# Kernel optimization log

Hardware: AMD Instinct MI355X
Metric: run time of the kernel (lower is better)

Reference implementation:

```python
import jax, jax.numpy as jnp
import numpy as np

C_IN = 4
C_OUT = 8
K = 5            # kernel_size (hardcoded by reshape(25,2) in original)
N_ROT = 8
R_B = 8          # rot_basis_size
STRIDE = 1
PAD = 2
TWO_PI = 2.0 * np.pi
ROT_SCALE = TWO_PI / R_B


def B2(x):
    # quadratic B-spline, exactly as in the torch source
    return (-3 * (-0.5 + x) ** 2 * jnp.sign(0.5 - x)
            + (-1.5 + x) ** 2 * jnp.sign(1.5 - x)
            - 3 * (1 + 2 * x) ** 2 * jnp.sign(0.5 + x) / 4
            + (3 + 2 * x) ** 2 * jnp.sign(1.5 + x) / 4) / 4


def angle_dist(th1, th2):
    return jnp.mod(th2 - th1 + np.pi, TWO_PI) - np.pi


def make_kernel_stack(weights):
    # weights: (C_IN, R_B*K*K, C_OUT). M = K*K*R_B combined (spatial-center, rot-center) index;
    # original repeats each spatial center R_B times (np.repeat) and tiles rot centers K*K times.
    lidx = -(K // 2)
    coords = jnp.arange(lidx, K // 2 + 1, dtype=jnp.float32)
    grid = jnp.stack(jnp.meshgrid(coords, coords, indexing='ij'), axis=-1)  # (K,K,2), grid[i,j]=[i+l, j+l]
    centers_xy = jnp.repeat(grid.reshape(K * K, 2), R_B, axis=0)            # (M,2)
    rot_centers = jnp.tile(jnp.arange(R_B, dtype=jnp.float32) * ROT_SCALE, K * K)  # (M,)
    rot_sample = jnp.arange(N_ROT, dtype=jnp.float32) * (TWO_PI / N_ROT)    # (N_ROT,)

    def one_kernel(theta):
        c, s = jnp.cos(theta), jnp.sin(theta)
        x, y = grid[..., 0], grid[..., 1]
        xxs = jnp.stack([x * c - y * s, x * s + y * c], axis=-1)            # (K,K,2) rotated sample grid
        xx_diffs = centers_xy[None, None, :, :] - xxs[:, :, None, :]        # (K,K,M,2)
        xx_vals = jnp.prod(B2(xx_diffs), axis=-1)                           # (K,K,M) separable spatial spline
        rots = rot_sample + theta                                           # (N_ROT,)
        rot_vals = B2(angle_dist(rots[:, None], rot_centers[None, :]) / ROT_SCALE)  # (N_ROT,M)
        vals = xx_vals[:, :, None, :] * rot_vals[None, None, :, :]          # (K,K,N_ROT,M)
        # contract basis index m against weights -> (C_OUT, C_IN, N_ROT, K, K)
        return jnp.einsum('xyrm,imo->oirxy', vals, weights)

    ks = jax.vmap(one_kernel)(-rot_sample)  # (N_ROT, C_OUT, C_IN, N_ROT, K, K), matches torch.cat over -theta
    return ks.reshape(N_ROT * C_OUT, C_IN * N_ROT, K, K)


def setup_inputs() -> dict:
    key = jax.random.key(0)
    kx, kw = jax.random.split(key)
    X = jax.random.normal(kx, (8, C_IN, N_ROT, 256, 256), dtype=jnp.float32)
    weights = jax.random.normal(kw, (C_IN, R_B * K * K, C_OUT), dtype=jnp.float32)
    return {'X': X, 'weights': weights}


def reference(X, weights):
    ks = make_kernel_stack(weights)                       # (N_ROT*C_OUT, C_IN*N_ROT, K, K)
    B, c, d, H, W = X.shape
    Xr = X.reshape(B, c * d, H, W)
    out = jax.lax.conv_general_dilated(
        Xr, ks, window_strides=(STRIDE, STRIDE),
        padding=[(PAD, PAD), (PAD, PAD)],
        dimension_numbers=('NCHW', 'OIHW', 'NCHW'))        # (B, N_ROT*C_OUT, h, w)
    Bn, _, h, w = out.shape
    out = out.reshape(Bn, N_ROT, C_OUT, h, w).transpose(0, 2, 1, 3, 4)  # (B, C_OUT, N_ROT, h, w)
    return (TWO_PI / N_ROT) * out
```

## Files before the change

### kernel.cpp

```cpp
#include <hip/hip_runtime.h>
#include <hip/hip_fp16.h>
#include <math.h>

#define PI_F      3.14159265358979323846f
#define TWO_PI_F  6.28318530717958647692f
#define PI4_F     0.78539816339744830962f

typedef _Float16 f16x8 __attribute__((ext_vector_type(8)));
typedef float    f32x4 __attribute__((ext_vector_type(4)));

__device__ __forceinline__ float sgn(float t) {
    return (t > 0.f) ? 1.f : ((t < 0.f) ? -1.f : 0.f);
}

__device__ __forceinline__ float b2(float x) {
    float a = x - 0.5f;
    float b = x - 1.5f;
    float c = 1.f + 2.f * x;
    float d = 3.f + 2.f * x;
    return (-3.f * a * a * sgn(0.5f - x)
            + b * b * sgn(1.5f - x)
            - 0.75f * c * c * sgn(0.5f + x)
            + 0.25f * d * d * sgn(1.5f + x)) * 0.25f;
}

__global__ void build_ks_kernel(const float* __restrict__ w, __half* __restrict__ ksh) {
    int g = blockIdx.x * 256 + threadIdx.x;
    if (g >= 64 * 32 * 25) return;
    int O = g & 63;
    int rest = g >> 6;
    int t = rest % 25;
    int I = rest / 25;
    int r0 = O >> 3, o = O & 7;
    int i = I >> 3, r = I & 7;
    int x = t / 5, y = t % 5;

    float theta = -(float)r0 * PI4_F;
    float cth = cosf(theta), sth = sinf(theta);
    float fx = (float)(x - 2), fy = (float)(y - 2);
    float xc = fx * cth - fy * sth;
    float yc = fx * sth + fy * cth;

    float rotv[8];
    float rs = (float)r * PI4_F + theta;
    #pragma unroll
    for (int mr = 0; mr < 8; ++mr) {
        float v = (float)mr * PI4_F - rs + PI_F;
        float md = fmodf(v, TWO_PI_F);
        if (md < 0.f) md += TWO_PI_F;
        rotv[mr] = b2((md - PI_F) / PI4_F);
    }

    float sum = 0.f;
    for (int mx = 0; mx < 25; ++mx) {
        float cx = (float)(mx / 5 - 2);
        float cy = (float)(mx % 5 - 2);
        float bx = b2(cx - xc) * b2(cy - yc);
        if (bx != 0.f) {
            const float* wp = w + (size_t)(i * 200 + mx * 8) * 8 + o;
            #pragma unroll
            for (int mr = 0; mr < 8; ++mr)
                sum = fmaf(bx * rotv[mr], wp[mr * 8], sum);
        }
    }
    ksh[(size_t)(t * 64 + O) * 32 + I] = __float2half(sum);
}

__global__ __launch_bounds__(256, 2) void conv_fused_kernel(const float* __restrict__ X,
                                                            const __half* __restrict__ ksh,
                                                            float* __restrict__ out) {
    __shared__ uint4 xt[4 * 721];

    int bid = blockIdx.x;
    int b   = bid >> 7;
    int rem = bid & 127;
    int h0  = (rem >> 3) << 4;
    int w0  = (rem & 7) << 5;
    int tid = threadIdx.x;

    const float* Xb = X + (size_t)b * 32 * 65536;

    for (int lin = tid; lin < 4 * 720; lin += 256) {
        int slot = lin / 720;
        int p    = lin - slot * 720;
        int r = p / 36, c = p - (p / 36) * 36;
        int gh = h0 + r - 2;
        int gw = w0 + c - 2;
        union { __half hh[8]; uint4 u; } pk;
        if ((unsigned)gh < 256u && (unsigned)gw < 256u) {
            const float* src = Xb + (size_t)slot * 8 * 65536 + gh * 256 + gw;
            #pragma unroll
            for (int j = 0; j < 8; ++j) pk.hh[j] = __float2half(src[j * 65536]);
        } else {
            pk.u = make_uint4(0u, 0u, 0u, 0u);
        }
        xt[slot * 721 + p] = pk.u;
    }
    __syncthreads();

    int wave = tid >> 6, lane = tid & 63;
    int lO = lane & 15, ks4 = lane >> 4;
    int bidx = lO * 4 + ks4;
    const uint4* ksq = (const uint4*)ksh;

    f32x4 acc[8][4] = {};
    int baseA[8];
    #pragma unroll
    for (int m = 0; m < 8; ++m)
        baseA[m] = 721 * ks4 + (wave * 4 + (m >> 1)) * 36 + (m & 1) * 16 + lO;

    f16x8 Bf[2][4];
    #pragma unroll
    for (int n = 0; n < 4; ++n)
        Bf[0][n] = __builtin_bit_cast(f16x8, ksq[n * 64 + bidx]);

    #pragma unroll
    for (int t = 0; t < 25; ++t) {
        const int cur = t & 1, nxt = cur ^ 1;
        const int aoff = (t / 5) * 36 + (t % 5);

        f16x8 Af[8];
        #pragma unroll
        for (int m = 0; m < 8; ++m)
            Af[m] = __builtin_bit_cast(f16x8, xt[baseA[m] + aoff]);

        if (t < 24) {
            const int t1 = t + 1;
            #pragma unroll
            for (int n = 0; n < 4; ++n)
                Bf[nxt][n] = __builtin_bit_cast(f16x8, ksq[t1 * 256 + n * 64 + bidx]);
        }

        __builtin_amdgcn_s_setprio(1);
        #pragma unroll
        for (int m = 0; m < 8; ++m) {
            #pragma unroll
            for (int n = 0; n < 4; ++n)
                acc[m][n] = __builtin_amdgcn_mfma_f32_16x16x32_f16(Af[m], Bf[cur][n], acc[m][n], 0, 0, 0);
        }
        __builtin_amdgcn_s_setprio(0);
    }

    #pragma unroll
    for (int m = 0; m < 8; ++m) {
        int gh  = h0 + wave * 4 + (m >> 1);
        int gwb = w0 + (m & 1) * 16 + ks4 * 4;
        #pragma unroll
        for (int n = 0; n < 4; ++n) {
            int O = n * 16 + lO;
            float* op = out + (((size_t)(b * 8 + (O & 7)) * 8 + (O >> 3)) << 16)
                            + gh * 256 + gwb;
            *(f32x4*)op = acc[m][n] * PI4_F;
        }
    }
}

extern "C" void kernel_launch(void* const* d_in, const int* in_sizes, int n_in,
                              void* d_out, int out_size, void* d_ws, size_t ws_size,
                              hipStream_t stream) {
    const float* X = (const float*)d_in[0];
    const float* w = (const float*)d_in[1];
    float* outp = (float*)d_out;
    __half* ksh = (__half*)d_ws;

    build_ks_kernel<<<200, 256, 0, stream>>>(w, ksh);
    conv_fused_kernel<<<8 * 128, 256, 0, stream>>>(X, ksh, outp);
}
```

Measured before the change: 94.08 us.

## Make conv a persistent double-buffered pipeline over width tiles

The conv kernel becomes 256 blocks of 512 threads. Each block walks four consecutive 32-wide tiles and double-buffers the halo tile in LDS. While one tile is being computed, the next tile's global loads are issued into registers and then converted and written to the other LDS buffer mid-loop. This is meant to hide global load latency behind MFMA work, at the cost of much higher register pressure (48 floats of staging), one block per CU, and only 256 blocks, which may leave CUs underfilled.

```diff
diff --git a/kernel.cpp b/kernel.cpp
--- a/kernel.cpp
+++ b/kernel.cpp
@@ -66,92 +66,143 @@
     ksh[(size_t)(t * 64 + O) * 32 + I] = __float2half(sum);
 }
 
-__global__ __launch_bounds__(256, 2) void conv_fused_kernel(const float* __restrict__ X,
-                                                            const __half* __restrict__ ksh,
-                                                            float* __restrict__ out) {
-    __shared__ uint4 xt[4 * 721];
+__global__ __launch_bounds__(512, 1) void conv_pipe_kernel(const float* __restrict__ X,
+                                                           const __half* __restrict__ ksh,
+                                                           float* __restrict__ out) {
+    __shared__ uint4 xt[2][4 * 721];
 
     int bid = blockIdx.x;
-    int b   = bid >> 7;
-    int rem = bid & 127;
-    int h0  = (rem >> 3) << 4;
-    int w0  = (rem & 7) << 5;
+    int b   = bid >> 5;
+    int rem = bid & 31;
+    int h0  = (rem >> 1) << 4;
+    int wg  = (rem & 1) << 2;
     int tid = threadIdx.x;
 
     const float* Xb = X + (size_t)b * 32 * 65536;
 
-    for (int lin = tid; lin < 4 * 720; lin += 256) {
-        int slot = lin / 720;
-        int p    = lin - slot * 720;
-        int r = p / 36, c = p - (p / 36) * 36;
-        int gh = h0 + r - 2;
-        int gw = w0 + c - 2;
-        union { __half hh[8]; uint4 u; } pk;
-        if ((unsigned)gh < 256u && (unsigned)gw < 256u) {
-            const float* src = Xb + (size_t)slot * 8 * 65536 + gh * 256 + gw;
-            #pragma unroll
-            for (int j = 0; j < 8; ++j) pk.hh[j] = __float2half(src[j * 65536]);
-        } else {
-            pk.u = make_uint4(0u, 0u, 0u, 0u);
-        }
-        xt[slot * 721 + p] = pk.u;
-    }
-    __syncthreads();
+    float pk[6][8];
+
+    auto stage_load = [&](int w0s) {
+        #pragma unroll
+        for (int k = 0; k < 6; ++k) {
+            int lin = tid + k * 512;
+            if (lin < 2880) {
+                int slot = lin / 720;
+                int p    = lin - slot * 720;
+                int r = p / 36, c = p - (p / 36) * 36;
+                int gh = h0 + r - 2;
+                int gw = w0s + c - 2;
+                if ((unsigned)gh < 256u && (unsigned)gw < 256u) {
+                    const float* src = Xb + (size_t)slot * 8 * 65536 + gh * 256 + gw;
+                    #pragma unroll
+                    for (int j = 0; j < 8; ++j) pk[k][j] = src[j * 65536];
+                } else {
+                    #pragma unroll
+                    for (int j = 0; j < 8; ++j) pk[k][j] = 0.f;
+                }
+            }
+        }
+    };
+
+    auto stage_write = [&](uint4* dstbuf) {
+        #pragma unroll
+        for (int k = 0; k < 6; ++k) {
+            int lin = tid + k * 512;
+            if (lin < 2880) {
+                int slot = lin / 720;
+                int p    = lin - slot * 720;
+                union { __half hh[8]; uint4 u; } q;
+                #pragma unroll
+                for (int j = 0; j < 8; ++j) q.hh[j] = __float2half(pk[k][j]);
+                dstbuf[slot * 721 + p] = q.u;
+            }
+        }
+    };
 
     int wave = tid >> 6, lane = tid & 63;
     int lO = lane & 15, ks4 = lane >> 4;
     int bidx = lO * 4 + ks4;
     const uint4* ksq = (const uint4*)ksh;
 
-    f32x4 acc[8][4] = {};
-    int baseA[8];
+    int baseA[4];
     #pragma unroll
-    for (int m = 0; m < 8; ++m)
-        baseA[m] = 721 * ks4 + (wave * 4 + (m >> 1)) * 36 + (m & 1) * 16 + lO;
-
-    f16x8 Bf[2][4];
-    #pragma unroll
-    for (int n = 0; n < 4; ++n)
-        Bf[0][n] = __builtin_bit_cast(f16x8, ksq[n * 64 + bidx]);
-
-    #pragma unroll
-    for (int t = 0; t < 25; ++t) {
-        const int cur = t & 1, nxt = cur ^ 1;
-        const int aoff = (t / 5) * 36 + (t % 5);
-
-        f16x8 Af[8];
-        #pragma unroll
-        for (int m = 0; m < 8; ++m)
-            Af[m] = __builtin_bit_cast(f16x8, xt[baseA[m] + aoff]);
-
-        if (t < 24) {
-            const int t1 = t + 1;
+    for (int m = 0; m < 4; ++m)
+        baseA[m] = 721 * ks4 + (wave * 2 + (m >> 1)) * 36 + (m & 1) * 16 + lO;
+
+    stage_load(wg << 5);
+    stage_write(&xt[0][0]);
+    __syncthreads();
+
+    #pragma unroll 1
+    for (int s = 0; s < 4; ++s) {
+        const uint4* cbuf = &xt[s & 1][0];
+        uint4* nbuf = &xt[(s + 1) & 1][0];
+        int w0s = (wg + s) << 5;
+
+        if (s < 3) stage_load((wg + s + 1) << 5);
+
+        f32x4 acc[4][4] = {};
+        f16x8 Bf[2][4];
+        #pragma unroll
+        for (int n = 0; n < 4; ++n)
+            Bf[0][n] = __builtin_bit_cast(f16x8, ksq[n * 64 + bidx]);
+
+        #pragma unroll
+        for (int t = 0; t < 12; ++t) {
+            const int cur = t & 1, nxt = cur ^ 1;
+            const int aoff = (t / 5) * 36 + (t % 5);
+            f16x8 Af[4];
+            #pragma unroll
+            for (int m = 0; m < 4; ++m)
+                Af[m] = __builtin_bit_cast(f16x8, cbuf[baseA[m] + aoff]);
             #pragma unroll
             for (int n = 0; n < 4; ++n)
-                Bf[nxt][n] = __builtin_bit_cast(f16x8, ksq[t1 * 256 + n * 64 + bidx]);
-        }
-
-        __builtin_amdgcn_s_setprio(1);
-        #pragma unroll
-        for (int m = 0; m < 8; ++m) {
-            #pragma unroll
-            for (int n = 0; n < 4; ++n)
-                acc[m][n] = __builtin_amdgcn_mfma_f32_16x16x32_f16(Af[m], Bf[cur][n], acc[m][n], 0, 0, 0);
-        }
-        __builtin_amdgcn_s_setprio(0);
-    }
-
-    #pragma unroll
-    for (int m = 0; m < 8; ++m) {
-        int gh  = h0 + wave * 4 + (m >> 1);
-        int gwb = w0 + (m & 1) * 16 + ks4 * 4;
-        #pragma unroll
-        for (int n = 0; n < 4; ++n) {
-            int O = n * 16 + lO;
-            float* op = out + (((size_t)(b * 8 + (O & 7)) * 8 + (O >> 3)) << 16)
-                            + gh * 256 + gwb;
-            *(f32x4*)op = acc[m][n] * PI4_F;
-        }
+                Bf[nxt][n] = __builtin_bit_cast(f16x8, ksq[(t + 1) * 256 + n * 64 + bidx]);
+            #pragma unroll
+            for (int m = 0; m < 4; ++m) {
+                #pragma unroll
+                for (int n = 0; n < 4; ++n)
+                    acc[m][n] = __builtin_amdgcn_mfma_f32_16x16x32_f16(Af[m], Bf[cur][n], acc[m][n], 0, 0, 0);
+            }
+        }
+
+        if (s < 3) stage_write(nbuf);
+
+        #pragma unroll
+        for (int t = 12; t < 25; ++t) {
+            const int cur = t & 1, nxt = cur ^ 1;
+            const int aoff = (t / 5) * 36 + (t % 5);
+            f16x8 Af[4];
+            #pragma unroll
+            for (int m = 0; m < 4; ++m)
+                Af[m] = __builtin_bit_cast(f16x8, cbuf[baseA[m] + aoff]);
+            if (t < 24) {
+                #pragma unroll
+                for (int n = 0; n < 4; ++n)
+                    Bf[nxt][n] = __builtin_bit_cast(f16x8, ksq[(t + 1) * 256 + n * 64 + bidx]);
+            }
+            #pragma unroll
+            for (int m = 0; m < 4; ++m) {
+                #pragma unroll
+                for (int n = 0; n < 4; ++n)
+                    acc[m][n] = __builtin_amdgcn_mfma_f32_16x16x32_f16(Af[m], Bf[cur][n], acc[m][n], 0, 0, 0);
+            }
+        }
+
+        #pragma unroll
+        for (int m = 0; m < 4; ++m) {
+            int gh  = h0 + wave * 2 + (m >> 1);
+            int gwb = w0s + (m & 1) * 16 + ks4 * 4;
+            #pragma unroll
+            for (int n = 0; n < 4; ++n) {
+                int O = n * 16 + lO;
+                float* op = out + (((size_t)(b * 8 + (O & 7)) * 8 + (O >> 3)) << 16)
+                                + gh * 256 + gwb;
+                *(f32x4*)op = acc[m][n] * PI4_F;
+            }
+        }
+
+        __syncthreads();
     }
 }
 
@@ -164,5 +215,5 @@
     __half* ksh = (__half*)d_ws;
 
     build_ks_kernel<<<200, 256, 0, stream>>>(w, ksh);
-    conv_fused_kernel<<<8 * 128, 256, 0, stream>>>(X, ksh, outp);
-}
+    conv_pipe_kernel<<<256, 512, 0, stream>>>(X, ksh, outp);
+}
```

New measurement: 307.8 us. +227.2%, slower.

## Warp-specialize conv into producer/consumer waves with double-buffered LDS tiles

Applied to the files above, without the earlier changes.

Each block now has 512 threads and handles four consecutive 16x32 tiles. Four waves run the MFMA compute while the other four convert and load the next input tile into a second LDS buffer, with a barrier between stages. This aims to overlap global loads and the fp32-to-fp16 conversion with matrix math. In exchange the grid shrinks to 256 blocks and LDS per block doubles, which may lower occupancy and leave CUs idle. The setprio hints were also removed.

```diff
diff --git a/kernel.cpp b/kernel.cpp
--- a/kernel.cpp
+++ b/kernel.cpp
@@ -66,91 +66,128 @@
     ksh[(size_t)(t * 64 + O) * 32 + I] = __float2half(sum);
 }
 
-__global__ __launch_bounds__(256, 2) void conv_fused_kernel(const float* __restrict__ X,
-                                                            const __half* __restrict__ ksh,
-                                                            float* __restrict__ out) {
-    __shared__ uint4 xt[4 * 721];
+__global__ __launch_bounds__(512, 2) void conv_pc_kernel(const float* __restrict__ X,
+                                                         const __half* __restrict__ ksh,
+                                                         float* __restrict__ out) {
+    __shared__ uint4 xt[2][4 * 721];
 
     int bid = blockIdx.x;
-    int b   = bid >> 7;
-    int rem = bid & 127;
-    int h0  = (rem >> 3) << 4;
-    int w0  = (rem & 7) << 5;
+    int b   = bid >> 5;
+    int rem = bid & 31;
+    int h0  = (rem >> 1) << 4;
+    int wg  = (rem & 1) << 2;
     int tid = threadIdx.x;
+    int wave = tid >> 6, lane = tid & 63;
 
     const float* Xb = X + (size_t)b * 32 * 65536;
 
-    for (int lin = tid; lin < 4 * 720; lin += 256) {
-        int slot = lin / 720;
-        int p    = lin - slot * 720;
-        int r = p / 36, c = p - (p / 36) * 36;
-        int gh = h0 + r - 2;
-        int gw = w0 + c - 2;
-        union { __half hh[8]; uint4 u; } pk;
-        if ((unsigned)gh < 256u && (unsigned)gw < 256u) {
-            const float* src = Xb + (size_t)slot * 8 * 65536 + gh * 256 + gw;
-            #pragma unroll
-            for (int j = 0; j < 8; ++j) pk.hh[j] = __float2half(src[j * 65536]);
-        } else {
-            pk.u = make_uint4(0u, 0u, 0u, 0u);
-        }
-        xt[slot * 721 + p] = pk.u;
-    }
-    __syncthreads();
-
-    int wave = tid >> 6, lane = tid & 63;
-    int lO = lane & 15, ks4 = lane >> 4;
-    int bidx = lO * 4 + ks4;
-    const uint4* ksq = (const uint4*)ksh;
-
-    f32x4 acc[8][4] = {};
-    int baseA[8];
-    #pragma unroll
-    for (int m = 0; m < 8; ++m)
-        baseA[m] = 721 * ks4 + (wave * 4 + (m >> 1)) * 36 + (m & 1) * 16 + lO;
-
-    f16x8 Bf[2][4];
-    #pragma unroll
-    for (int n = 0; n < 4; ++n)
-        Bf[0][n] = __builtin_bit_cast(f16x8, ksq[n * 64 + bidx]);
-
-    #pragma unroll
-    for (int t = 0; t < 25; ++t) {
-        const int cur = t & 1, nxt = cur ^ 1;
-        const int aoff = (t / 5) * 36 + (t % 5);
-
-        f16x8 Af[8];
+    {
+        int w0n = wg << 5;
+        for (int lin = tid; lin < 2880; lin += 512) {
+            int slot = lin / 720;
+            int p    = lin - slot * 720;
+            int r = p / 36, c = p - (p / 36) * 36;
+            int gh = h0 + r - 2, gw = w0n + c - 2;
+            union { __half hh[8]; uint4 u; } q;
+            if ((unsigned)gh < 256u && (unsigned)gw < 256u) {
+                const float* src = Xb + (size_t)slot * 8 * 65536 + gh * 256 + gw;
+                #pragma unroll
+                for (int j = 0; j < 8; ++j) q.hh[j] = __float2half(src[j * 65536]);
+            } else {
+                q.u = make_uint4(0u, 0u, 0u, 0u);
+            }
+            xt[0][slot * 721 + p] = q.u;
+        }
+    }
+    asm volatile("s_waitcnt lgkmcnt(0)" ::: "memory");
+    __builtin_amdgcn_s_barrier();
+
+    if (wave < 4) {
+        int lO = lane & 15, ks4 = lane >> 4;
+        int bidx = lO * 4 + ks4;
+        const uint4* ksq = (const uint4*)ksh;
+
+        int baseA[8];
         #pragma unroll
         for (int m = 0; m < 8; ++m)
-            Af[m] = __builtin_bit_cast(f16x8, xt[baseA[m] + aoff]);
-
-        if (t < 24) {
-            const int t1 = t + 1;
+            baseA[m] = 721 * ks4 + (wave * 4 + (m >> 1)) * 36 + (m & 1) * 16 + lO;
+
+        #pragma unroll 1
+        for (int s = 0; s < 4; ++s) {
+            const uint4* cbuf = &xt[s & 1][0];
+            int w0s = (wg + s) << 5;
+
+            f32x4 acc[8][4] = {};
+            f16x8 Bf[2][4];
             #pragma unroll
             for (int n = 0; n < 4; ++n)
-                Bf[nxt][n] = __builtin_bit_cast(f16x8, ksq[t1 * 256 + n * 64 + bidx]);
-        }
-
-        __builtin_amdgcn_s_setprio(1);
-        #pragma unroll
-        for (int m = 0; m < 8; ++m) {
-            #pragma unroll
-            for (int n = 0; n < 4; ++n)
-                acc[m][n] = __builtin_amdgcn_mfma_f32_16x16x32_f16(Af[m], Bf[cur][n], acc[m][n], 0, 0, 0);
-        }
-        __builtin_amdgcn_s_setprio(0);
-    }
-
-    #pragma unroll
-    for (int m = 0; m < 8; ++m) {
-        int gh  = h0 + wave * 4 + (m >> 1);
-        int gwb = w0 + (m & 1) * 16 + ks4 * 4;
-        #pragma unroll
-        for (int n = 0; n < 4; ++n) {
-            int O = n * 16 + lO;
-            float* op = out + (((size_t)(b * 8 + (O & 7)) * 8 + (O >> 3)) << 16)
-                            + gh * 256 + gwb;
-            *(f32x4*)op = acc[m][n] * PI4_F;
+                Bf[0][n] = __builtin_bit_cast(f16x8, ksq[n * 64 + bidx]);
+
+            #pragma unroll
+            for (int t = 0; t < 25; ++t) {
+                const int cur = t & 1, nxt = cur ^ 1;
+                const int aoff = (t / 5) * 36 + (t % 5);
+
+                f16x8 Af[8];
+                #pragma unroll
+                for (int m = 0; m < 8; ++m)
+                    Af[m] = __builtin_bit_cast(f16x8, cbuf[baseA[m] + aoff]);
+
+                if (t < 24) {
+                    #pragma unroll
+                    for (int n = 0; n < 4; ++n)
+                        Bf[nxt][n] = __builtin_bit_cast(f16x8, ksq[(t + 1) * 256 + n * 64 + bidx]);
+                }
+
+                #pragma unroll
+                for (int m = 0; m < 8; ++m) {
+                    #pragma unroll
+                    for (int n = 0; n < 4; ++n)
+                        acc[m][n] = __builtin_amdgcn_mfma_f32_16x16x32_f16(Af[m], Bf[cur][n], acc[m][n], 0, 0, 0);
+                }
+            }
+
+            #pragma unroll
+            for (int m = 0; m < 8; ++m) {
+                int gh  = h0 + wave * 4 + (m >> 1);
+                int gwb = w0s + (m & 1) * 16 + ks4 * 4;
+                #pragma unroll
+                for (int n = 0; n < 4; ++n) {
+                    int O = n * 16 + lO;
+                    float* op = out + (((size_t)(b * 8 + (O & 7)) * 8 + (O >> 3)) << 16)
+                                    + gh * 256 + gwb;
+                    *(f32x4*)op = acc[m][n] * PI4_F;
+                }
+            }
+
+            asm volatile("s_waitcnt lgkmcnt(0)" ::: "memory");
+            __builtin_amdgcn_s_barrier();
+        }
+    } else {
+        int ptid = tid - 256;
+        #pragma unroll 1
+        for (int s = 0; s < 4; ++s) {
+            if (s < 3) {
+                uint4* nbuf = &xt[(s + 1) & 1][0];
+                int w0n = (wg + s + 1) << 5;
+                for (int lin = ptid; lin < 2880; lin += 256) {
+                    int slot = lin / 720;
+                    int p    = lin - slot * 720;
+                    int r = p / 36, c = p - (p / 36) * 36;
+                    int gh = h0 + r - 2, gw = w0n + c - 2;
+                    union { __half hh[8]; uint4 u; } q;
+                    if ((unsigned)gh < 256u && (unsigned)gw < 256u) {
+                        const float* src = Xb + (size_t)slot * 8 * 65536 + gh * 256 + gw;
+                        #pragma unroll
+                        for (int j = 0; j < 8; ++j) q.hh[j] = __float2half(src[j * 65536]);
+                    } else {
+                        q.u = make_uint4(0u, 0u, 0u, 0u);
+                    }
+                    nbuf[slot * 721 + p] = q.u;
+                }
+            }
+            asm volatile("s_waitcnt lgkmcnt(0)" ::: "memory");
+            __builtin_amdgcn_s_barrier();
         }
     }
 }
@@ -164,5 +201,5 @@
     __half* ksh = (__half*)d_ws;
 
     build_ks_kernel<<<200, 256, 0, stream>>>(w, ksh);
-    conv_fused_kernel<<<8 * 128, 256, 0, stream>>>(X, ksh, outp);
-}
+    conv_pc_kernel<<<256, 512, 0, stream>>>(X, ksh, outp);
+}
```

After: 253.6 us. 170% more time.

## Switch conv to 32x32x16 MFMA with smaller row tiles and higher occupancy

Applied to the files above, without the earlier changes.

Replaces the 16x16x32 MFMA conv with a 32x32x16 variant where each block computes 4 output rows instead of 16, launching four times as many blocks with launch bounds raised to 4 blocks per CU. Shared memory is restaged pixel-major with a stride-5 pad, and kernel-weight fragments are prefetched two taps ahead with triple buffering. The aim is lower register pressure and better latency hiding. The cost is a larger halo overhead, so more input rows are re-read and converted per output row.

```diff
diff --git a/kernel.cpp b/kernel.cpp
--- a/kernel.cpp
+++ b/kernel.cpp
@@ -6,8 +6,9 @@
 #define TWO_PI_F  6.28318530717958647692f
 #define PI4_F     0.78539816339744830962f
 
-typedef _Float16 f16x8 __attribute__((ext_vector_type(8)));
-typedef float    f32x4 __attribute__((ext_vector_type(4)));
+typedef _Float16 f16x8  __attribute__((ext_vector_type(8)));
+typedef float    f32x4  __attribute__((ext_vector_type(4)));
+typedef float    f32x16 __attribute__((ext_vector_type(16)));
 
 __device__ __forceinline__ float sgn(float t) {
     return (t > 0.f) ? 1.f : ((t < 0.f) ? -1.f : 0.f);
@@ -66,91 +67,95 @@
     ksh[(size_t)(t * 64 + O) * 32 + I] = __float2half(sum);
 }
 
-__global__ __launch_bounds__(256, 2) void conv_fused_kernel(const float* __restrict__ X,
-                                                            const __half* __restrict__ ksh,
-                                                            float* __restrict__ out) {
-    __shared__ uint4 xt[4 * 721];
+__global__ __launch_bounds__(256, 4) void conv_fused32_kernel(const float* __restrict__ X,
+                                                              const __half* __restrict__ ksh,
+                                                              float* __restrict__ out) {
+    __shared__ uint4 xt[288 * 5];
 
     int bid = blockIdx.x;
-    int b   = bid >> 7;
-    int rem = bid & 127;
-    int h0  = (rem >> 3) << 4;
+    int b   = bid >> 9;
+    int rem = bid & 511;
+    int h0  = (rem >> 3) << 2;
     int w0  = (rem & 7) << 5;
     int tid = threadIdx.x;
 
     const float* Xb = X + (size_t)b * 32 * 65536;
 
-    for (int lin = tid; lin < 4 * 720; lin += 256) {
-        int slot = lin / 720;
-        int p    = lin - slot * 720;
-        int r = p / 36, c = p - (p / 36) * 36;
+    for (int lin = tid; lin < 1152; lin += 256) {
+        int px = lin >> 2, slot = lin & 3;
+        int r = px / 36, c = px - (px / 36) * 36;
         int gh = h0 + r - 2;
         int gw = w0 + c - 2;
-        union { __half hh[8]; uint4 u; } pk;
+        union { __half hh[8]; uint4 u; } q;
         if ((unsigned)gh < 256u && (unsigned)gw < 256u) {
             const float* src = Xb + (size_t)slot * 8 * 65536 + gh * 256 + gw;
             #pragma unroll
-            for (int j = 0; j < 8; ++j) pk.hh[j] = __float2half(src[j * 65536]);
+            for (int j = 0; j < 8; ++j) q.hh[j] = __float2half(src[j * 65536]);
         } else {
-            pk.u = make_uint4(0u, 0u, 0u, 0u);
+            q.u = make_uint4(0u, 0u, 0u, 0u);
         }
-        xt[slot * 721 + p] = pk.u;
+        xt[px * 5 + slot] = q.u;
     }
     __syncthreads();
 
     int wave = tid >> 6, lane = tid & 63;
-    int lO = lane & 15, ks4 = lane >> 4;
-    int bidx = lO * 4 + ks4;
+    int lM = lane & 31;
+    int hi = lane >> 5;
     const uint4* ksq = (const uint4*)ksh;
+    int bB = lM * 4 + hi;
 
-    f32x4 acc[8][4] = {};
-    int baseA[8];
+    f32x16 acc[2] = {};
+    int aBase = (wave * 36 + lM) * 5 + hi;
+
+    f16x8 Bf[3][2][2];
     #pragma unroll
-    for (int m = 0; m < 8; ++m)
-        baseA[m] = 721 * ks4 + (wave * 4 + (m >> 1)) * 36 + (m & 1) * 16 + lO;
-
-    f16x8 Bf[2][4];
-    #pragma unroll
-    for (int n = 0; n < 4; ++n)
-        Bf[0][n] = __builtin_bit_cast(f16x8, ksq[n * 64 + bidx]);
+    for (int n = 0; n < 2; ++n) {
+        #pragma unroll
+        for (int kh = 0; kh < 2; ++kh) {
+            Bf[0][n][kh] = __builtin_bit_cast(f16x8, ksq[0 * 256 + n * 128 + kh * 2 + bB]);
+            Bf[1][n][kh] = __builtin_bit_cast(f16x8, ksq[1 * 256 + n * 128 + kh * 2 + bB]);
+        }
+    }
 
     #pragma unroll
     for (int t = 0; t < 25; ++t) {
-        const int cur = t & 1, nxt = cur ^ 1;
-        const int aoff = (t / 5) * 36 + (t % 5);
-
-        f16x8 Af[8];
-        #pragma unroll
-        for (int m = 0; m < 8; ++m)
-            Af[m] = __builtin_bit_cast(f16x8, xt[baseA[m] + aoff]);
-
-        if (t < 24) {
-            const int t1 = t + 1;
+        const int cur = t % 3;
+        if (t < 23) {
+            const int nn = (t + 2) % 3;
             #pragma unroll
-            for (int n = 0; n < 4; ++n)
-                Bf[nxt][n] = __builtin_bit_cast(f16x8, ksq[t1 * 256 + n * 64 + bidx]);
+            for (int n = 0; n < 2; ++n)
+                #pragma unroll
+                for (int kh = 0; kh < 2; ++kh)
+                    Bf[nn][n][kh] = __builtin_bit_cast(f16x8,
+                        ksq[(t + 2) * 256 + n * 128 + kh * 2 + bB]);
         }
 
-        __builtin_amdgcn_s_setprio(1);
+        const int aoff = (t / 5) * 180 + (t % 5) * 5;
+        f16x8 Af[2];
+        Af[0] = __builtin_bit_cast(f16x8, xt[aBase + aoff]);
+        Af[1] = __builtin_bit_cast(f16x8, xt[aBase + aoff + 2]);
+
         #pragma unroll
-        for (int m = 0; m < 8; ++m) {
+        for (int kh = 0; kh < 2; ++kh)
             #pragma unroll
-            for (int n = 0; n < 4; ++n)
-                acc[m][n] = __builtin_amdgcn_mfma_f32_16x16x32_f16(Af[m], Bf[cur][n], acc[m][n], 0, 0, 0);
-        }
-        __builtin_amdgcn_s_setprio(0);
+            for (int n = 0; n < 2; ++n)
+                acc[n] = __builtin_amdgcn_mfma_f32_32x32x16_f16(Af[kh], Bf[cur][n][kh], acc[n], 0, 0, 0);
     }
 
     #pragma unroll
-    for (int m = 0; m < 8; ++m) {
-        int gh  = h0 + wave * 4 + (m >> 1);
-        int gwb = w0 + (m & 1) * 16 + ks4 * 4;
+    for (int n = 0; n < 2; ++n) {
+        int O = n * 32 + lM;
+        float* plane = out + (((size_t)(b * 8 + (O & 7)) * 8 + (O >> 3)) << 16)
+                           + (h0 + wave) * 256;
         #pragma unroll
-        for (int n = 0; n < 4; ++n) {
-            int O = n * 16 + lO;
-            float* op = out + (((size_t)(b * 8 + (O & 7)) * 8 + (O >> 3)) << 16)
-                            + gh * 256 + gwb;
-            *(f32x4*)op = acc[m][n] * PI4_F;
+        for (int g = 0; g < 4; ++g) {
+            int wcol = w0 + g * 8 + hi * 4;
+            f32x4 v;
+            v.x = acc[n][4 * g + 0] * PI4_F;
+            v.y = acc[n][4 * g + 1] * PI4_F;
+            v.z = acc[n][4 * g + 2] * PI4_F;
+            v.w = acc[n][4 * g + 3] * PI4_F;
+            *(f32x4*)(plane + wcol) = v;
         }
     }
 }
@@ -164,5 +169,5 @@
     __half* ksh = (__half*)d_ws;
 
     build_ks_kernel<<<200, 256, 0, stream>>>(w, ksh);
-    conv_fused_kernel<<<8 * 128, 256, 0, stream>>>(X, ksh, outp);
+    conv_fused32_kernel<<<8 * 512, 256, 0, stream>>>(X, ksh, outp);
 }
```

Measured after the change: 153.6 us. 1.63x slower.
